# Kernel optimization log

Hardware: AMD Instinct MI355X
Metric: run time of the kernel (lower is better)

## Reference

```python
import jax, jax.numpy as jnp
import numpy as np
import math

N_GENES_TOTAL = 5000   # full gene table (fragments.n_genes)
N_CELLS_TOTAL = 10000  # full cell count (libsize buffer)
NBINS = 128            # spline components per gene
N_LATENT = 64
B = 256                # n_cells in minibatch
G = 2000               # genes_oi
NCUTS = 500_000


def setup_inputs() -> dict:
    key = jax.random.key(0)
    ks = jax.random.split(key, 12)
    latent = jax.random.normal(ks[0], (B, N_LATENT), jnp.float32)
    genes_oi = jax.random.randint(ks[1], (G,), 0, N_GENES_TOTAL)
    cells_oi = jax.random.randint(ks[2], (B,), 0, N_CELLS_TOTAL)
    cut_coordinates = jax.random.uniform(ks[3], (NCUTS,), jnp.float32)
    cut_local_cellxgene_ix = jax.random.randint(ks[4], (NCUTS,), 0, B * G)
    cut_local_gene_ix = jax.random.randint(ks[5], (NCUTS,), 0, G)
    local_cellxgene_ix = jax.random.randint(ks[6], (NCUTS,), 0, B * G)
    s = 1.0 / math.sqrt(N_LATENT)
    logit_weight = jax.random.uniform(ks[7], (N_GENES_TOTAL, N_LATENT, NBINS), jnp.float32, -s, s)
    rho_weight = jax.random.uniform(ks[8], (N_GENES_TOTAL, N_LATENT), jnp.float32, -s / 100.0, s / 100.0)
    rho_bias = jax.random.uniform(ks[9], (N_GENES_TOTAL,), jnp.float32, 1e-4, 1e-2)
    libsize = jax.random.randint(ks[10], (N_CELLS_TOTAL,), 1000, 20000)
    spline_heights = 0.01 * jax.random.normal(ks[11], (N_GENES_TOTAL, NBINS), jnp.float32)
    return {
        "latent": latent, "genes_oi": genes_oi, "cells_oi": cells_oi,
        "cut_coordinates": cut_coordinates,
        "cut_local_cellxgene_ix": cut_local_cellxgene_ix,
        "cut_local_gene_ix": cut_local_gene_ix,
        "local_cellxgene_ix": local_cellxgene_ix,
        "logit_weight": logit_weight, "rho_weight": rho_weight,
        "rho_bias": rho_bias, "libsize": libsize,
        "spline_heights": spline_heights,
        "n_cells": B, "n_genes": G,
    }


def reference(latent, genes_oi, cells_oi, cut_coordinates,
              cut_local_cellxgene_ix, cut_local_gene_ix, local_cellxgene_ix,
              logit_weight, rho_weight, rho_bias, libsize, spline_heights,
              n_cells, n_genes):
    # Decoder with n_layers=0: nn is identity
    lw = logit_weight[genes_oi]                     # [G, L, C]
    rw = rho_weight[genes_oi]                       # [G, L]
    mixture_delta = jnp.einsum('bl,glc->bgc', latent, lw)   # [B, G, C]
    rho_delta = latent @ rw.T                       # [B, G]

    # gather per-cut mixture deltas
    delta_flat = mixture_delta.reshape(n_cells * n_genes, -1)
    delta_cut = delta_flat[cut_local_cellxgene_ix]  # [Ncuts, C]

    # spline/mixture log-likelihood: per-gene histogram density with delta
    gene_heights = spline_heights[genes_oi]         # [G, C]
    h = gene_heights[cut_local_gene_ix] + delta_cut  # [Ncuts, C]
    logp_bins = jax.nn.log_softmax(h, axis=-1)
    nbins = h.shape[-1]
    bin_ix = jnp.clip((cut_coordinates * nbins).astype(jnp.int32), 0, nbins - 1)
    likelihood_mixture = (
        jnp.take_along_axis(logp_bins, bin_ix[:, None], axis=-1)[:, 0]
        + jnp.log(jnp.float32(nbins))
    )

    # Poisson fragment-count likelihood
    rate = (rho_bias[genes_oi][None, :] * jnp.exp(rho_delta)
            * libsize[cells_oi].astype(jnp.float32)[:, None])   # [B, G]
    counts = jnp.bincount(local_cellxgene_ix, length=n_cells * n_genes)
    counts = counts.reshape(n_cells, n_genes).astype(jnp.float32)
    ll_counts = counts * jnp.log(rate) - rate - jax.scipy.special.gammaln(counts + 1.0)

    likelihood = likelihood_mixture.sum() + ll_counts.sum()
    return -likelihood
```

## Files before the change

### kernel.cpp

```cpp
#include <hip/hip_runtime.h>

#define LDIM 64
#define CDIM 128
#define NREP 8
#define SUBCAP 64
#define MAXPER (NREP * SUBCAP)
#define LOG128 4.8520302639196171f

typedef __attribute__((ext_vector_type(8))) short bfrag;
typedef __attribute__((ext_vector_type(4))) float f32x4;

static __device__ __forceinline__ unsigned short f2bf(float f) {
    unsigned int x = __float_as_uint(f);
    unsigned int r = (x + 0x7fffu + ((x >> 16) & 1u)) >> 16;
    return (unsigned short)r;
}
static __device__ __forceinline__ float bf2f(unsigned int u) {
    return __uint_as_float(u << 16);
}

__global__ __launch_bounds__(256) void zero_kernel(uint4* __restrict__ p, size_t n16,
                                                   float* __restrict__ out, int out_size) {
    size_t i = (size_t)blockIdx.x * blockDim.x + threadIdx.x;
    size_t stride = (size_t)gridDim.x * blockDim.x;
    for (; i < n16; i += stride) p[i] = make_uint4(0u, 0u, 0u, 0u);
    if (blockIdx.x == 0 && threadIdx.x < (unsigned)out_size) out[threadIdx.x] = 0.f;
}

__global__ __launch_bounds__(256) void prep1_kernel(
    const float* __restrict__ heights, unsigned short* __restrict__ hbf, int nheights,
    const float* __restrict__ latent, unsigned short* __restrict__ latbf, int nlat,
    const int* __restrict__ cut_pair, const int* __restrict__ cut_gene,
    const float* __restrict__ coord, const int* __restrict__ genes_oi,
    const int* __restrict__ local_cxg, unsigned int* __restrict__ cnt_rep,
    unsigned int* __restrict__ bucket, unsigned int* __restrict__ countsT,
    int ncuts, int B, int G, int N, unsigned int magicG) {
    int stride = gridDim.x * blockDim.x;
    int rep = blockIdx.x & (NREP - 1);
    for (int i = blockIdx.x * blockDim.x + threadIdx.x; i < N; i += stride) {
        if (i < nheights) hbf[i] = f2bf(heights[i]);
        if (i < nlat) latbf[i] = f2bf(latent[i]);
        if (i < ncuts) {
            unsigned int p = (unsigned int)cut_pair[i];
            unsigned int cell = __umulhi(p, magicG);
            unsigned int g = p - cell * (unsigned int)G;
            unsigned int gg = (unsigned int)genes_oi[cut_gene[i]];
            int bin = (int)(coord[i] * 128.0f);
            bin = min(max(bin, 0), 127);
            unsigned int slot = atomicAdd(&cnt_rep[rep * G + (int)g], 1u);
            if (slot < SUBCAP)
                bucket[(size_t)g * MAXPER + rep * SUBCAP + slot] =
                    (cell << 24) | (gg << 7) | (unsigned int)bin;
            unsigned int q = (unsigned int)local_cxg[i];
            unsigned int cell2 = __umulhi(q, magicG);
            unsigned int g2 = q - cell2 * (unsigned int)G;
            atomicAdd(&countsT[(size_t)g2 * (unsigned int)B + cell2], 1u);
        }
    }
}

__global__ __launch_bounds__(512) void prep2_kernel(
    const float* __restrict__ lw, const int* __restrict__ genes_oi,
    unsigned short* __restrict__ lwT, int G) {
    __shared__ float s[LDIM][CDIM + 1];
    int g = blockIdx.x, t = threadIdx.x;
    int gene = genes_oi[g];
    const float4* src = (const float4*)(lw + (size_t)gene * LDIM * CDIM);
    #pragma unroll
    for (int it = 0; it < 4; ++it) {
        int idx = t + it * 512;
        int k = idx >> 5, nq = idx & 31;
        float4 v = src[idx];
        s[k][nq * 4 + 0] = v.x; s[k][nq * 4 + 1] = v.y;
        s[k][nq * 4 + 2] = v.z; s[k][nq * 4 + 3] = v.w;
    }
    __syncthreads();
    #pragma unroll
    for (int it = 0; it < 2; ++it) {
        int idx = t + it * 512;
        int n = idx >> 3, kq = idx & 7;
        union { unsigned short u[8]; uint4 q; } pk;
        #pragma unroll
        for (int j = 0; j < 8; ++j) pk.u[j] = f2bf(s[kq * 8 + j][n]);
        *(uint4*)(lwT + ((size_t)g * CDIM + n) * LDIM + kq * 8) = pk.q;
    }
}

__global__ __launch_bounds__(512, 2) void fused_kernel(
    const float* __restrict__ latent, const unsigned short* __restrict__ latbf,
    const int* __restrict__ genes_oi, const unsigned short* __restrict__ lwT,
    const unsigned short* __restrict__ hbf, const unsigned int* __restrict__ bucket,
    const unsigned int* __restrict__ cnt_rep, const unsigned int* __restrict__ countsT,
    const int* __restrict__ cells_oi,
    const float* __restrict__ rho_weight, const float* __restrict__ rho_bias,
    const int* __restrict__ libsize, int B, int G, float* __restrict__ out) {
    __shared__ unsigned short dlds[256 * CDIM];
    __shared__ unsigned int clds[MAXPER];
    __shared__ float red[8];
    int t = threadIdx.x;
    int g = blockIdx.x;
    int gene = genes_oi[g];
    int wv = t >> 6, ln = t & 63;
    int l15 = ln & 15, l4 = ln >> 4;
    float accs = 0.f;

    unsigned int cs[NREP + 1];
    cs[0] = 0;
    #pragma unroll
    for (int r = 0; r < NREP; ++r)
        cs[r + 1] = cs[r] + min(cnt_rep[r * G + g], (unsigned)SUBCAP);

    {
        const unsigned int* bk = bucket + (size_t)g * MAXPER;
        #pragma unroll
        for (int r = 0; r < NREP; ++r) {
            unsigned int base = cs[r], cr = cs[r + 1] - base;
            for (unsigned int i = (unsigned int)t; i < cr; i += 512u)
                clds[base + i] = bk[r * SUBCAP + i];
        }
    }

    {
        f32x4 acc[2][8];
        #pragma unroll
        for (int m = 0; m < 2; ++m)
            #pragma unroll
            for (int q = 0; q < 8; ++q) acc[m][q] = (f32x4){0.f, 0.f, 0.f, 0.f};
        #pragma unroll
        for (int ks = 0; ks < 2; ++ks) {
            int kk = ks * 32 + l4 * 8;
            bfrag a0 = *(const bfrag*)(latbf + (wv * 32 + l15) * LDIM + kk);
            bfrag a1 = *(const bfrag*)(latbf + (wv * 32 + 16 + l15) * LDIM + kk);
            #pragma unroll
            for (int q = 0; q < 8; ++q) {
                int col = q * 16 + l15;
                bfrag b = *(const bfrag*)(lwT + ((size_t)g * CDIM + col) * LDIM + kk);
                acc[0][q] = __builtin_amdgcn_mfma_f32_16x16x32_bf16(a0, b, acc[0][q], 0, 0, 0);
                acc[1][q] = __builtin_amdgcn_mfma_f32_16x16x32_bf16(a1, b, acc[1][q], 0, 0, 0);
            }
        }
        #pragma unroll
        for (int m = 0; m < 2; ++m)
            #pragma unroll
            for (int q = 0; q < 8; ++q)
                #pragma unroll
                for (int r = 0; r < 4; ++r) {
                    int row = wv * 32 + m * 16 + l4 * 4 + r;
                    int col = q * 16 + l15;
                    dlds[row * CDIM + (col ^ ((row & 7) * 8))] = f2bf(acc[m][q][r]);
                }
    }
    __syncthreads();

    {
        unsigned int C = cs[NREP];
        int grp = t >> 3, sub = t & 7;
        for (unsigned int i = (unsigned int)grp; i < C; i += 64u) {
            unsigned int rc = clds[i];
            int row = (int)(rc >> 24);
            unsigned int gg = (rc >> 7) & 0x1FFFu;
            int sw = (row & 7) * 8;
            uint4 dva = *(const uint4*)(dlds + row * CDIM + ((sub * 16) ^ sw));
            uint4 dvb = *(const uint4*)(dlds + row * CDIM + ((sub * 16 + 8) ^ sw));
            const uint4* hp = (const uint4*)(hbf + ((size_t)gg << 7) + sub * 16);
            uint4 hva = hp[0], hvb = hp[1];
            float h0  = bf2f(hva.x & 0xffffu) + bf2f(dva.x & 0xffffu);
            float h1  = bf2f(hva.x >> 16)     + bf2f(dva.x >> 16);
            float h2  = bf2f(hva.y & 0xffffu) + bf2f(dva.y & 0xffffu);
            float h3  = bf2f(hva.y >> 16)     + bf2f(dva.y >> 16);
            float h4  = bf2f(hva.z & 0xffffu) + bf2f(dva.z & 0xffffu);
            float h5  = bf2f(hva.z >> 16)     + bf2f(dva.z >> 16);
            float h6  = bf2f(hva.w & 0xffffu) + bf2f(dva.w & 0xffffu);
            float h7  = bf2f(hva.w >> 16)     + bf2f(dva.w >> 16);
            float h8  = bf2f(hvb.x & 0xffffu) + bf2f(dvb.x & 0xffffu);
            float h9  = bf2f(hvb.x >> 16)     + bf2f(dvb.x >> 16);
            float h10 = bf2f(hvb.y & 0xffffu) + bf2f(dvb.y & 0xffffu);
            float h11 = bf2f(hvb.y >> 16)     + bf2f(dvb.y >> 16);
            float h12 = bf2f(hvb.z & 0xffffu) + bf2f(dvb.z & 0xffffu);
            float h13 = bf2f(hvb.z >> 16)     + bf2f(dvb.z >> 16);
            float h14 = bf2f(hvb.w & 0xffffu) + bf2f(dvb.w & 0xffffu);
            float h15 = bf2f(hvb.w >> 16)     + bf2f(dvb.w >> 16);
            float s = __expf(h0)  + __expf(h1)  + __expf(h2)  + __expf(h3)
                    + __expf(h4)  + __expf(h5)  + __expf(h6)  + __expf(h7)
                    + __expf(h8)  + __expf(h9)  + __expf(h10) + __expf(h11)
                    + __expf(h12) + __expf(h13) + __expf(h14) + __expf(h15);
            #pragma unroll
            for (int o = 1; o < 8; o <<= 1) s += __shfl_xor(s, o);
            int bin = (int)(rc & 127u);
            int e = bin & 15;
            float sel = h0;
            sel = (e == 1)  ? h1  : sel;
            sel = (e == 2)  ? h2  : sel;
            sel = (e == 3)  ? h3  : sel;
            sel = (e == 4)  ? h4  : sel;
            sel = (e == 5)  ? h5  : sel;
            sel = (e == 6)  ? h6  : sel;
            sel = (e == 7)  ? h7  : sel;
            sel = (e == 8)  ? h8  : sel;
            sel = (e == 9)  ? h9  : sel;
            sel = (e == 10) ? h10 : sel;
            sel = (e == 11) ? h11 : sel;
            sel = (e == 12) ? h12 : sel;
            sel = (e == 13) ? h13 : sel;
            sel = (e == 14) ? h14 : sel;
            sel = (e == 15) ? h15 : sel;
            float hsel = __shfl(sel, (ln & 56) | (bin >> 4));
            if (sub == 0) accs += hsel - __logf(s) + LOG128;
        }
    }

    if (t < 256) {
        const float4* la = (const float4*)(latent + (size_t)t * LDIM);
        const float4* rw = (const float4*)(rho_weight + (size_t)gene * LDIM);
        float d = 0.f;
        #pragma unroll
        for (int k = 0; k < LDIM / 4; ++k) {
            float4 a = la[k], w = rw[k];
            d += a.x * w.x + a.y * w.y + a.z * w.z + a.w * w.w;
        }
        float rb = rho_bias[gene];
        float lib = (float)libsize[cells_oi[t]];
        float lrate = __logf(rb) + d + __logf(lib);
        float rate = __expf(lrate);
        unsigned int c = countsT[(size_t)g * B + t];
        float lgam = 0.f;
        for (unsigned int k = 2; k <= c; ++k) lgam += __logf((float)k);
        accs += (float)c * lrate - rate - lgam;
    }

    #pragma unroll
    for (int o = 32; o; o >>= 1) accs += __shfl_xor(accs, o);
    if (ln == 0) red[wv] = accs;
    __syncthreads();
    if (t == 0) {
        float s = red[0] + red[1] + red[2] + red[3] + red[4] + red[5] + red[6] + red[7];
        atomicAdd(out, -s);
    }
}

extern "C" void kernel_launch(void* const* d_in, const int* in_sizes, int n_in,
                              void* d_out, int out_size, void* d_ws, size_t ws_size,
                              hipStream_t stream) {
    const float* latent         = (const float*)d_in[0];
    const int*   genes_oi       = (const int*)d_in[1];
    const int*   cells_oi       = (const int*)d_in[2];
    const float* cut_coord      = (const float*)d_in[3];
    const int*   cut_pair       = (const int*)d_in[4];
    const int*   cut_gene       = (const int*)d_in[5];
    const int*   local_cxg      = (const int*)d_in[6];
    const float* logit_weight   = (const float*)d_in[7];
    const float* rho_weight     = (const float*)d_in[8];
    const float* rho_bias       = (const float*)d_in[9];
    const int*   libsize        = (const int*)d_in[10];
    const float* spline_heights = (const float*)d_in[11];
    int G = in_sizes[1];
    int B = in_sizes[2];
    int ncuts = in_sizes[4];
    int nheights = in_sizes[11];
    int nlat = B * LDIM;
    unsigned int magicG = (unsigned int)((0x100000000ULL + (unsigned)G - 1) / (unsigned)G);

    char* ws = (char*)d_ws;
    size_t off = 0;
    unsigned int* countsT = (unsigned int*)(ws + off);
    off += ((size_t)B * G * 4 + 255) & ~(size_t)255;
    unsigned int* cnt_rep = (unsigned int*)(ws + off);
    off += ((size_t)G * NREP * 4 + 255) & ~(size_t)255;
    size_t zero_bytes = off;
    unsigned int* bucket = (unsigned int*)(ws + off);
    off += ((size_t)G * MAXPER * 4 + 255) & ~(size_t)255;
    unsigned short* lwT = (unsigned short*)(ws + off);
    off += ((size_t)G * CDIM * LDIM * 2 + 255) & ~(size_t)255;
    unsigned short* hbf = (unsigned short*)(ws + off);
    off += ((size_t)nheights * 2 + 255) & ~(size_t)255;
    unsigned short* latbf = (unsigned short*)(ws + off);
    off += ((size_t)nlat * 2 + 255) & ~(size_t)255;

    float* out = (float*)d_out;
    zero_kernel<<<1024, 256, 0, stream>>>((uint4*)ws, zero_bytes / 16, out, out_size);

    int N = ncuts > nheights ? ncuts : nheights;
    prep1_kernel<<<2048, 256, 0, stream>>>(
        spline_heights, hbf, nheights, latent, latbf, nlat,
        cut_pair, cut_gene, cut_coord, genes_oi, local_cxg,
        cnt_rep, bucket, countsT, ncuts, B, G, N, magicG);
    prep2_kernel<<<G, 512, 0, stream>>>(logit_weight, genes_oi, lwT, G);
    fused_kernel<<<G, 512, 0, stream>>>(
        latent, latbf, genes_oi, lwT, hbf, bucket,
        cnt_rep, countsT, cells_oi,
        rho_weight, rho_bias, libsize, B, G, out);
}
```

Before: 145.3 us.

## Fold workspace zeroing into prep2, transpose MFMA epilogue, raise fused occupancy

Removes the separate zero kernel and has the lw transpose kernel also zero the counters and output, launching it before prep1 so one launch disappears. The MFMA operands are swapped so each lane holds four consecutive columns, which lets the epilogue write packed 64-bit bf16 pairs to LDS instead of scalar 16-bit stores. The bf16 pack now truncates instead of rounding. Launch bounds of the fused kernel go from 2 to 4 blocks per CU, which may force register spills.

```diff
diff --git a/kernel.cpp b/kernel.cpp
--- a/kernel.cpp
+++ b/kernel.cpp
@@ -18,13 +18,39 @@
 static __device__ __forceinline__ float bf2f(unsigned int u) {
     return __uint_as_float(u << 16);
 }
-
-__global__ __launch_bounds__(256) void zero_kernel(uint4* __restrict__ p, size_t n16,
-                                                   float* __restrict__ out, int out_size) {
-    size_t i = (size_t)blockIdx.x * blockDim.x + threadIdx.x;
-    size_t stride = (size_t)gridDim.x * blockDim.x;
-    for (; i < n16; i += stride) p[i] = make_uint4(0u, 0u, 0u, 0u);
-    if (blockIdx.x == 0 && threadIdx.x < (unsigned)out_size) out[threadIdx.x] = 0.f;
+static __device__ __forceinline__ unsigned int pack2(float hi, float lo) {
+    return (__float_as_uint(hi) & 0xffff0000u) | (__float_as_uint(lo) >> 16);
+}
+
+__global__ __launch_bounds__(512) void prep2_kernel(
+    const float* __restrict__ lw, const int* __restrict__ genes_oi,
+    unsigned short* __restrict__ lwT, uint4* __restrict__ zp, size_t zn16,
+    float* __restrict__ out, int out_size, int G) {
+    __shared__ float s[LDIM][CDIM + 1];
+    int g = blockIdx.x, t = threadIdx.x;
+    for (size_t zi = (size_t)g * 512 + t; zi < zn16; zi += (size_t)gridDim.x * 512)
+        zp[zi] = make_uint4(0u, 0u, 0u, 0u);
+    if (g == 0 && t < out_size) out[t] = 0.f;
+    int gene = genes_oi[g];
+    const float4* src = (const float4*)(lw + (size_t)gene * LDIM * CDIM);
+    #pragma unroll
+    for (int it = 0; it < 4; ++it) {
+        int idx = t + it * 512;
+        int k = idx >> 5, nq = idx & 31;
+        float4 v = src[idx];
+        s[k][nq * 4 + 0] = v.x; s[k][nq * 4 + 1] = v.y;
+        s[k][nq * 4 + 2] = v.z; s[k][nq * 4 + 3] = v.w;
+    }
+    __syncthreads();
+    #pragma unroll
+    for (int it = 0; it < 2; ++it) {
+        int idx = t + it * 512;
+        int n = idx >> 3, kq = idx & 7;
+        union { unsigned short u[8]; uint4 q; } pk;
+        #pragma unroll
+        for (int j = 0; j < 8; ++j) pk.u[j] = f2bf(s[kq * 8 + j][n]);
+        *(uint4*)(lwT + ((size_t)g * CDIM + n) * LDIM + kq * 8) = pk.q;
+    }
 }
 
 __global__ __launch_bounds__(256) void prep1_kernel(
@@ -59,34 +85,7 @@
     }
 }
 
-__global__ __launch_bounds__(512) void prep2_kernel(
-    const float* __restrict__ lw, const int* __restrict__ genes_oi,
-    unsigned short* __restrict__ lwT, int G) {
-    __shared__ float s[LDIM][CDIM + 1];
-    int g = blockIdx.x, t = threadIdx.x;
-    int gene = genes_oi[g];
-    const float4* src = (const float4*)(lw + (size_t)gene * LDIM * CDIM);
-    #pragma unroll
-    for (int it = 0; it < 4; ++it) {
-        int idx = t + it * 512;
-        int k = idx >> 5, nq = idx & 31;
-        float4 v = src[idx];
-        s[k][nq * 4 + 0] = v.x; s[k][nq * 4 + 1] = v.y;
-        s[k][nq * 4 + 2] = v.z; s[k][nq * 4 + 3] = v.w;
-    }
-    __syncthreads();
-    #pragma unroll
-    for (int it = 0; it < 2; ++it) {
-        int idx = t + it * 512;
-        int n = idx >> 3, kq = idx & 7;
-        union { unsigned short u[8]; uint4 q; } pk;
-        #pragma unroll
-        for (int j = 0; j < 8; ++j) pk.u[j] = f2bf(s[kq * 8 + j][n]);
-        *(uint4*)(lwT + ((size_t)g * CDIM + n) * LDIM + kq * 8) = pk.q;
-    }
-}
-
-__global__ __launch_bounds__(512, 2) void fused_kernel(
+__global__ __launch_bounds__(512, 4) void fused_kernel(
     const float* __restrict__ latent, const unsigned short* __restrict__ latbf,
     const int* __restrict__ genes_oi, const unsigned short* __restrict__ lwT,
     const unsigned short* __restrict__ hbf, const unsigned int* __restrict__ bucket,
@@ -129,26 +128,27 @@
         #pragma unroll
         for (int ks = 0; ks < 2; ++ks) {
             int kk = ks * 32 + l4 * 8;
-            bfrag a0 = *(const bfrag*)(latbf + (wv * 32 + l15) * LDIM + kk);
-            bfrag a1 = *(const bfrag*)(latbf + (wv * 32 + 16 + l15) * LDIM + kk);
+            bfrag lat0 = *(const bfrag*)(latbf + (wv * 32 + l15) * LDIM + kk);
+            bfrag lat1 = *(const bfrag*)(latbf + (wv * 32 + 16 + l15) * LDIM + kk);
             #pragma unroll
             for (int q = 0; q < 8; ++q) {
-                int col = q * 16 + l15;
-                bfrag b = *(const bfrag*)(lwT + ((size_t)g * CDIM + col) * LDIM + kk);
-                acc[0][q] = __builtin_amdgcn_mfma_f32_16x16x32_bf16(a0, b, acc[0][q], 0, 0, 0);
-                acc[1][q] = __builtin_amdgcn_mfma_f32_16x16x32_bf16(a1, b, acc[1][q], 0, 0, 0);
+                bfrag lwf = *(const bfrag*)(lwT + ((size_t)g * CDIM + q * 16 + l15) * LDIM + kk);
+                acc[0][q] = __builtin_amdgcn_mfma_f32_16x16x32_bf16(lwf, lat0, acc[0][q], 0, 0, 0);
+                acc[1][q] = __builtin_amdgcn_mfma_f32_16x16x32_bf16(lwf, lat1, acc[1][q], 0, 0, 0);
             }
         }
         #pragma unroll
-        for (int m = 0; m < 2; ++m)
-            #pragma unroll
-            for (int q = 0; q < 8; ++q)
-                #pragma unroll
-                for (int r = 0; r < 4; ++r) {
-                    int row = wv * 32 + m * 16 + l4 * 4 + r;
-                    int col = q * 16 + l15;
-                    dlds[row * CDIM + (col ^ ((row & 7) * 8))] = f2bf(acc[m][q][r]);
-                }
+        for (int m = 0; m < 2; ++m) {
+            int cl = wv * 32 + m * 16 + l15;
+            int sx = (cl & 7) << 3;
+            #pragma unroll
+            for (int q = 0; q < 8; ++q) {
+                unsigned int p0 = pack2(acc[m][q][1], acc[m][q][0]);
+                unsigned int p1 = pack2(acc[m][q][3], acc[m][q][2]);
+                int colx = (q * 16 + l4 * 4) ^ sx;
+                *(uint2*)(dlds + cl * CDIM + colx) = make_uint2(p0, p1);
+            }
+        }
     }
     __syncthreads();
 
@@ -159,7 +159,7 @@
             unsigned int rc = clds[i];
             int row = (int)(rc >> 24);
             unsigned int gg = (rc >> 7) & 0x1FFFu;
-            int sw = (row & 7) * 8;
+            int sw = (row & 7) << 3;
             uint4 dva = *(const uint4*)(dlds + row * CDIM + ((sub * 16) ^ sw));
             uint4 dvb = *(const uint4*)(dlds + row * CDIM + ((sub * 16 + 8) ^ sw));
             const uint4* hp = (const uint4*)(hbf + ((size_t)gg << 7) + sub * 16);
@@ -277,14 +277,13 @@
     off += ((size_t)nlat * 2 + 255) & ~(size_t)255;
 
     float* out = (float*)d_out;
-    zero_kernel<<<1024, 256, 0, stream>>>((uint4*)ws, zero_bytes / 16, out, out_size);
-
     int N = ncuts > nheights ? ncuts : nheights;
+    prep2_kernel<<<G, 512, 0, stream>>>(logit_weight, genes_oi, lwT,
+                                        (uint4*)ws, zero_bytes / 16, out, out_size, G);
     prep1_kernel<<<2048, 256, 0, stream>>>(
         spline_heights, hbf, nheights, latent, latbf, nlat,
         cut_pair, cut_gene, cut_coord, genes_oi, local_cxg,
         cnt_rep, bucket, countsT, ncuts, B, G, N, magicG);
-    prep2_kernel<<<G, 512, 0, stream>>>(logit_weight, genes_oi, lwT, G);
     fused_kernel<<<G, 512, 0, stream>>>(
         latent, latbf, genes_oi, lwT, hbf, bucket,
         cnt_rep, countsT, cells_oi,
```

Measured after the change: 139.4 us. 1.04x faster.
